# Optimization experiments

Measured on AMD Instinct MI355X. Metric: run time of the kernel, lower is better.

Reference implementation:

```python
import jax, jax.numpy as jnp
import numpy as np


def setup_inputs() -> dict:
    key = jax.random.key(0)
    k1, k2, k3, k4, k5 = jax.random.split(key, 5)
    N, M, K = 200000, 50, 4
    T = 1000.0
    ti = jnp.sort(jax.random.uniform(k1, (N,), dtype=jnp.float32) * T)
    mi = jax.random.randint(k2, (N,), 0, M, dtype=jnp.int64)
    mu_at_events = jax.random.uniform(k3, (N,), dtype=jnp.float32) * 0.5 + 0.05
    alpha = jax.random.uniform(k4, (K, M, M), dtype=jnp.float32) * 0.1
    gamma = jax.random.uniform(k5, (K,), dtype=jnp.float32) * 2.0 + 0.5
    return {"ti": ti, "mi": mi, "mu_at_events": mu_at_events, "alpha": alpha, "gamma": gamma}


def _hawkes_logsum(ti, mi, mu_at_events, alpha, gamma):
    # ti: [N] sorted event times; mi: [N] event types in [0, M)
    # alpha: [K, M, M]; gamma: [K]; mu_at_events: [N]
    N = ti.shape[0]
    M = alpha.shape[1]
    # inter-event gaps; dt[0] = 0 so the first event has zero excitation state
    dt = jnp.concatenate([jnp.zeros((1,), ti.dtype), ti[1:] - ti[:-1]])  # [N]
    a = jnp.exp(-gamma[None, :] * dt[:, None])  # [N, K] decay factors
    # one-hot of the PREVIOUS event's type (row 0 is all-zero, matching e_mi)
    prev_onehot = jnp.zeros((N, M), ti.dtype).at[jnp.arange(1, N), mi[:-1]].set(1.0)
    b = a[:, None, :] * prev_onehot[:, :, None]  # [N, M, K]

    # linear recurrence S_i = a_i * S_{i-1} + b_i via associative scan
    # combine((a1,b1),(a2,b2)) = (a1*a2, a2*b1 + b2)
    def combine(x, y):
        a1, b1 = x
        a2, b2 = y
        return (a1 * a2, a2[:, None, :] * b1 + b2)

    _, S = jax.lax.associative_scan(combine, (a, b))  # S: [N, M, K]
    # S[i, m, k] = sum_{j < i, m_j = m} exp(-gamma_k (t_i - t_j))
    alpha_at = alpha[:, mi, :]  # [K, N, M] rows of alpha for each event's type
    lam = mu_at_events + jnp.einsum('knm,nmk,k->n', alpha_at, S, gamma)  # [N]
    return jnp.sum(jnp.log(lam))


def reference(ti, mi, mu_at_events, alpha, gamma):
    return _hawkes_logsum(ti, mi, mu_at_events, alpha, gamma)
```

## Files before the change

### kernel.cpp

```cpp
#include <hip/hip_runtime.h>

#define CHUNK 256
#define MM 50
#define KK 4
#define STATE (MM*KK)
#define ASTRIDE 51
#define SUP 32
#define NSMAX 26
#define SUBSZ 32
#define GMAX 1024

__device__ int      g_ticket;
__device__ unsigned g_flag[GMAX];
__device__ unsigned g_sflag[64];
__device__ float    g_chunkB[GMAX * STATE];
__device__ float    g_superB[64 * STATE];

__device__ __forceinline__ unsigned short f2bf(float x) {
  unsigned u = __float_as_uint(x);
  u += 0x7fffu + ((u >> 16) & 1u);
  return (unsigned short)(u >> 16);
}
__device__ __forceinline__ float bflo(unsigned u) { return __uint_as_float(u << 16); }
__device__ __forceinline__ float bfhi(unsigned u) { return __uint_as_float(u & 0xffff0000u); }

__device__ __forceinline__ void st_agent(float* p, float v) {
  __hip_atomic_store(p, v, __ATOMIC_RELAXED, __HIP_MEMORY_SCOPE_AGENT);
}
__device__ __forceinline__ float ld_agent(const float* p) {
  return __hip_atomic_load(p, __ATOMIC_RELAXED, __HIP_MEMORY_SCOPE_AGENT);
}
__device__ __forceinline__ void spin_flag(unsigned* p, unsigned want) {
  while (__hip_atomic_load(p, __ATOMIC_RELAXED, __HIP_MEMORY_SCOPE_AGENT) != want)
    __builtin_amdgcn_s_sleep(2);
}

__global__ __launch_bounds__(512) void hawkes_fused(
    const float* __restrict__ ti, const int* __restrict__ mi,
    const float* __restrict__ mu, const float* __restrict__ alpha,
    const float* __restrict__ gamma, float* __restrict__ out,
    int N, int G, int NB) {
  int tid = threadIdx.x;
  __shared__ int vid_s;
  __shared__ uint2 P[MM * ASTRIDE];
  __shared__ __align__(16) float4 Fj[2 * CHUNK];
  __shared__ int   cj[2 * CHUNK];
  __shared__ __align__(16) float Q[16][STATE];
  __shared__ float red8[8];
  __shared__ float teL[SUP];
  __shared__ float tlast[NSMAX];
  __shared__ float SldsA[STATE];
  __shared__ float SldsB[STATE];
  __shared__ __align__(16) float RA[MM * 20];
  __shared__ __align__(16) float RB[MM * 20];

  if (tid == 0) vid_s = atomicAdd(&g_ticket, 1);

  int b = blockIdx.x;
  int gA = 2 * b, gB = gA + 1;
  bool hasB = (gB < G);
  int lA = gA * CHUNK;
  int sup = gA / SUP;
  int g0c = sup * SUP;
  int half = tid >> 8;
  int cidx = tid & 255;

  float gk0 = gamma[0], gk1 = gamma[1], gk2 = gamma[2], gk3 = gamma[3];
  float gkc = (tid & 2) ? ((tid & 1) ? gk3 : gk2) : ((tid & 1) ? gk1 : gk0);

  for (int i = tid; i < 16 * STATE; i += 512) ((float*)Q)[i] = 0.f;

  if (tid < SUP) {
    int c = g0c + tid;
    if (c < G) teL[tid] = ti[min(N, (c + 1) * CHUNK) - 1];
  } else if (tid >= 64 && tid < 64 + NSMAX) {
    int s = tid - 64;
    if (s < sup) tlast[s] = ti[min(N, (s + 1) * SUP * CHUNK) - 1];
  }

  float t_refA = ti[(gA == 0) ? 0 : (lA - 1)];
  float t_refB = ti[min(N, lA + CHUNK) - 1];
  float t_ref = half ? t_refB : t_refA;

  int j = lA - 1 + tid;
  int rX = min(N, lA + (half + 1) * CHUNK);
  bool valid = (j >= 0) && (j <= rX - 2);
  int myc = 0;
  float4 myF = make_float4(0.f, 0.f, 0.f, 0.f);
  if (valid) {
    myc = mi[j];
    float tj = ti[j] - t_ref;
    myF = make_float4(__expf(gk0 * tj), __expf(gk1 * tj),
                      __expf(gk2 * tj), __expf(gk3 * tj));
  }
  cj[tid] = myc;
  Fj[tid] = myF;
  __syncthreads();

  if (valid) {
    float* q = &Q[tid >> 5][myc * KK];
    atomicAdd(q + 0, myF.x); atomicAdd(q + 1, myF.y);
    atomicAdd(q + 2, myF.z); atomicAdd(q + 3, myF.w);
  }
  __syncthreads();

  bool sumr = (cidx < STATE) && (half == 0 || hasB);
  int gX = half ? gB : gA;
  float Bv = 0.f, dX = 0.f;
  if (sumr) {
    float tot = 0.f;
    #pragma unroll
    for (int q = 0; q < 8; ++q) tot += Q[half * 8 + q][cidx];
    dX = __expf(-gkc * (teL[gX - g0c] - t_ref));
    Bv = dX * tot;
    st_agent(&g_chunkB[(size_t)gX * STATE + cidx], Bv);
    float run = 0.f;
    #pragma unroll
    for (int q = 0; q < 8; ++q) {
      float tq = Q[half * 8 + q][cidx];
      Q[half * 8 + q][cidx] = run;
      run += tq;
    }
  }
  if (b == 0 && tid == 0) st_agent(out, 0.f);
  __syncthreads();
  unsigned DONE = (unsigned)(vid_s / NB) + 1u;
  if (tid == 0) {
    asm volatile("s_waitcnt vmcnt(0)" ::: "memory");
    __hip_atomic_store(&g_flag[gA], DONE, __ATOMIC_RELAXED, __HIP_MEMORY_SCOPE_AGENT);
    if (hasB)
      __hip_atomic_store(&g_flag[gB], DONE, __ATOMIC_RELAXED, __HIP_MEMORY_SCOPE_AGENT);
  }

  for (int idx = tid; idx < MM * MM; idx += 512) {
    int c = idx / MM, cp = idx - c * MM;
    float a0 = gk0 * alpha[idx];
    float a1 = gk1 * alpha[2500 + idx];
    float a2 = gk2 * alpha[5000 + idx];
    float a3 = gk3 * alpha[7500 + idx];
    P[c * ASTRIDE + cp] =
        make_uint2((unsigned)f2bf(a0) | ((unsigned)f2bf(a1) << 16),
                   (unsigned)f2bf(a2) | ((unsigned)f2bf(a3) << 16));
  }

  int n = lA + tid;
  bool en = (n < N);
  int c_n = en ? mi[n] : 0;
  float tn = 0.f, mun = 0.f;
  if (en) { tn = ti[n] - t_ref; mun = mu[n]; }

  int nlocA = gA - g0c;
  bool closer = (hasB && (gB - g0c == SUP - 1)) || (b == NB - 1);
  float S = 0.f;

  if (closer) {
    if (tid < nlocA) spin_flag(&g_flag[g0c + tid], DONE);
    __syncthreads();
    if (tid < STATE) {
      #pragma unroll 16
      for (int u = 0; u < nlocA; ++u)
        S += __expf(-gkc * (t_refA - teL[u])) * ld_agent(&g_chunkB[(size_t)(g0c + u) * STATE + tid]);
      SldsB[tid] = dX * S + Bv;
    }
    __syncthreads();
    if (sumr && half) {
      st_agent(&g_superB[(size_t)sup * STATE + cidx], dX * SldsB[cidx] + Bv);
    }
    __syncthreads();
    if (tid == 0) {
      asm volatile("s_waitcnt vmcnt(0)" ::: "memory");
      __hip_atomic_store(&g_sflag[sup], DONE, __ATOMIC_RELAXED, __HIP_MEMORY_SCOPE_AGENT);
    }
  }
  __syncthreads();

  float4 acc = make_float4(0.f, 0.f, 0.f, 0.f);
  if (en) {
    int rowb = c_n * ASTRIDE;
    const float4* wb = (const float4*)&Q[tid >> 5][0];
    if (cidx >= SUBSZ) {
      #pragma unroll 10
      for (int m = 0; m < MM; ++m) {
        uint2 p = P[rowb + m];
        float4 w = wb[m];
        acc.x += bflo(p.x) * w.x; acc.y += bfhi(p.x) * w.y;
        acc.z += bflo(p.y) * w.z; acc.w += bfhi(p.y) * w.w;
      }
    }
    int base = tid & ~(SUBSZ - 1);
    #pragma unroll 4
    for (int s = base; s <= tid; ++s) {
      uint2 p = P[rowb + cj[s]];
      float4 f = Fj[s];
      acc.x += bflo(p.x) * f.x; acc.y += bfhi(p.x) * f.y;
      acc.z += bflo(p.y) * f.z; acc.w += bfhi(p.y) * f.w;
    }
  }

  if (!closer) {
    if (tid < nlocA) spin_flag(&g_flag[g0c + tid], DONE);
    __syncthreads();
    if (tid < STATE) {
      #pragma unroll 16
      for (int u = 0; u < nlocA; ++u)
        S += __expf(-gkc * (t_refA - teL[u])) * ld_agent(&g_chunkB[(size_t)(g0c + u) * STATE + tid]);
    }
  }
  if (tid < sup) spin_flag(&g_sflag[tid], DONE);
  __syncthreads();
  if (tid < STATE) {
    #pragma unroll 16
    for (int s = 0; s < sup; ++s)
      S += __expf(-gkc * (t_refA - tlast[s])) * ld_agent(&g_superB[(size_t)s * STATE + tid]);
    SldsA[tid] = S;
    SldsB[tid] = dX * S + Bv;
  }
  __syncthreads();

  if (sumr) {
    int c = cidx >> 2, k = cidx & 3;
    const float* Sx = half ? SldsB : SldsA;
    float rv = 0.f;
    #pragma unroll 10
    for (int m = 0; m < MM; ++m) {
      uint2 p = P[c * ASTRIDE + m];
      unsigned w = (k & 2) ? p.y : p.x;
      float pv = (k & 1) ? bfhi(w) : bflo(w);
      rv += pv * Sx[m * KK + k];
    }
    (half ? RB : RA)[c * 20 + k] = rv;
  }
  __syncthreads();

  float local = 0.f;
  if (en) {
    const float* Rx = half ? RB : RA;
    float4 rv = *(const float4*)&Rx[c_n * 20];
    float lam = mun
              + __expf(-gk0 * tn) * (acc.x + rv.x)
              + __expf(-gk1 * tn) * (acc.y + rv.y)
              + __expf(-gk2 * tn) * (acc.z + rv.z)
              + __expf(-gk3 * tn) * (acc.w + rv.w);
    local = __logf(lam);
  }
  #pragma unroll
  for (int off = 32; off > 0; off >>= 1)
    local += __shfl_down(local, off, 64);
  if ((tid & 63) == 0) red8[tid >> 6] = local;
  __syncthreads();
  if (tid == 0) {
    float acc8 = 0.f;
    #pragma unroll
    for (int w = 0; w < 8; ++w) acc8 += red8[w];
    atomicAdd(out, acc8);
  }
}

extern "C" void kernel_launch(void* const* d_in, const int* in_sizes, int n_in,
                              void* d_out, int out_size, void* d_ws, size_t ws_size,
                              hipStream_t stream) {
  const float* ti    = (const float*)d_in[0];
  const int*   mi    = (const int*)d_in[1];
  const float* mu    = (const float*)d_in[2];
  const float* alpha = (const float*)d_in[3];
  const float* gamma = (const float*)d_in[4];
  float* out = (float*)d_out;
  int N = in_sizes[0];
  int G = (N + CHUNK - 1) / CHUNK;
  if (G > GMAX) return;
  int NB = (G + 1) / 2;

  hawkes_fused<<<NB, 512, 0, stream>>>(ti, mi, mu, alpha, gamma, out, N, G, NB);
}
```

Baseline: 88.70 us.

## Process four chunks per block with two events per thread

Each 512-thread block now handles four 256-event chunks instead of two, with every thread processing two events. The in-block chunk prefix is chained serially through shared memory, which halves the block count and the number of cross-block flag handshakes in the decoupled lookback. In exchange each block does more serial work and uses more LDS and registers, which may cut occupancy and parallelism (about 196 blocks for 256 CUs).

```diff
diff --git a/kernel.cpp b/kernel.cpp
--- a/kernel.cpp
+++ b/kernel.cpp
@@ -3,11 +3,11 @@
 #define CHUNK 256
 #define MM 50
 #define KK 4
-#define STATE (MM*KK)
+#define STATE 200
 #define ASTRIDE 51
 #define SUP 32
 #define NSMAX 26
-#define SUBSZ 32
+#define QUAD 4
 #define GMAX 1024
 
 __device__ int      g_ticket;
@@ -35,7 +35,7 @@
     __builtin_amdgcn_s_sleep(2);
 }
 
-__global__ __launch_bounds__(512) void hawkes_fused(
+__global__ __launch_bounds__(512) void hawkes_quad(
     const float* __restrict__ ti, const int* __restrict__ mi,
     const float* __restrict__ mu, const float* __restrict__ alpha,
     const float* __restrict__ gamma, float* __restrict__ out,
@@ -43,32 +43,29 @@
   int tid = threadIdx.x;
   __shared__ int vid_s;
   __shared__ uint2 P[MM * ASTRIDE];
-  __shared__ __align__(16) float4 Fj[2 * CHUNK];
-  __shared__ int   cj[2 * CHUNK];
-  __shared__ __align__(16) float Q[16][STATE];
-  __shared__ float red8[8];
+  __shared__ __align__(16) float4 Fj[4 * CHUNK];
+  __shared__ int   cj[4 * CHUNK];
+  __shared__ __align__(16) float Q[32][STATE];
+  __shared__ float BvL[QUAD][STATE];
+  __shared__ float Slds[QUAD][STATE];
+  __shared__ __align__(16) float RQ[QUAD][MM * 20];
   __shared__ float teL[SUP];
   __shared__ float tlast[NSMAX];
-  __shared__ float SldsA[STATE];
-  __shared__ float SldsB[STATE];
-  __shared__ __align__(16) float RA[MM * 20];
-  __shared__ __align__(16) float RB[MM * 20];
+  __shared__ float red8[8];
 
   if (tid == 0) vid_s = atomicAdd(&g_ticket, 1);
 
   int b = blockIdx.x;
-  int gA = 2 * b, gB = gA + 1;
-  bool hasB = (gB < G);
-  int lA = gA * CHUNK;
-  int sup = gA / SUP;
+  int c0 = b * QUAD;
+  int lQ = c0 * CHUNK;
+  int nEx = min(QUAD, G - c0);
+  int sup = b >> 3;
   int g0c = sup * SUP;
-  int half = tid >> 8;
-  int cidx = tid & 255;
+  int nloc = c0 - g0c;
 
   float gk0 = gamma[0], gk1 = gamma[1], gk2 = gamma[2], gk3 = gamma[3];
-  float gkc = (tid & 2) ? ((tid & 1) ? gk3 : gk2) : ((tid & 1) ? gk1 : gk0);
-
-  for (int i = tid; i < 16 * STATE; i += 512) ((float*)Q)[i] = 0.f;
+
+  for (int i = tid; i < 32 * STATE; i += 512) ((float*)Q)[i] = 0.f;
 
   if (tid < SUP) {
     int c = g0c + tid;
@@ -78,48 +75,62 @@
     if (s < sup) tlast[s] = ti[min(N, (s + 1) * SUP * CHUNK) - 1];
   }
 
-  float t_refA = ti[(gA == 0) ? 0 : (lA - 1)];
-  float t_refB = ti[min(N, lA + CHUNK) - 1];
-  float t_ref = half ? t_refB : t_refA;
-
-  int j = lA - 1 + tid;
-  int rX = min(N, lA + (half + 1) * CHUNK);
-  bool valid = (j >= 0) && (j <= rX - 2);
-  int myc = 0;
-  float4 myF = make_float4(0.f, 0.f, 0.f, 0.f);
-  if (valid) {
-    myc = mi[j];
-    float tj = ti[j] - t_ref;
-    myF = make_float4(__expf(gk0 * tj), __expf(gk1 * tj),
+  float tref0 = ti[(b == 0) ? 0 : (lQ - 1)];
+
+  int   myc[2]; float4 myF[2]; bool vld[2]; float trefE[2];
+  #pragma unroll
+  for (int ev = 0; ev < 2; ++ev) {
+    int slot = tid + 512 * ev;
+    int ch = slot >> 8;
+    int j = lQ - 1 + slot;
+    int rch = min(N, lQ + (ch + 1) * CHUNK);
+    int tri = (b == 0 && ch == 0) ? 0 : (lQ + ch * CHUNK - 1);
+    trefE[ev] = ti[min(N - 1, tri)];
+    bool v = (j >= 0) && (j <= rch - 2);
+    int c = 0; float4 F = make_float4(0.f, 0.f, 0.f, 0.f);
+    if (v) {
+      c = mi[j];
+      float tj = ti[j] - trefE[ev];
+      F = make_float4(__expf(gk0 * tj), __expf(gk1 * tj),
                       __expf(gk2 * tj), __expf(gk3 * tj));
-  }
-  cj[tid] = myc;
-  Fj[tid] = myF;
-  __syncthreads();
-
-  if (valid) {
-    float* q = &Q[tid >> 5][myc * KK];
-    atomicAdd(q + 0, myF.x); atomicAdd(q + 1, myF.y);
-    atomicAdd(q + 2, myF.z); atomicAdd(q + 3, myF.w);
-  }
-  __syncthreads();
-
-  bool sumr = (cidx < STATE) && (half == 0 || hasB);
-  int gX = half ? gB : gA;
-  float Bv = 0.f, dX = 0.f;
-  if (sumr) {
-    float tot = 0.f;
-    #pragma unroll
-    for (int q = 0; q < 8; ++q) tot += Q[half * 8 + q][cidx];
-    dX = __expf(-gkc * (teL[gX - g0c] - t_ref));
-    Bv = dX * tot;
-    st_agent(&g_chunkB[(size_t)gX * STATE + cidx], Bv);
-    float run = 0.f;
-    #pragma unroll
-    for (int q = 0; q < 8; ++q) {
-      float tq = Q[half * 8 + q][cidx];
-      Q[half * 8 + q][cidx] = run;
-      run += tq;
+    }
+    myc[ev] = c; myF[ev] = F; vld[ev] = v;
+    cj[slot] = c; Fj[slot] = F;
+  }
+  __syncthreads();
+
+  #pragma unroll
+  for (int ev = 0; ev < 2; ++ev) {
+    if (vld[ev]) {
+      int slot = tid + 512 * ev;
+      float* q = &Q[slot >> 5][myc[ev] * KK];
+      atomicAdd(q + 0, myF[ev].x); atomicAdd(q + 1, myF[ev].y);
+      atomicAdd(q + 2, myF[ev].z); atomicAdd(q + 3, myF[ev].w);
+    }
+  }
+  __syncthreads();
+
+  #pragma unroll
+  for (int half = 0; half < 2; ++half) {
+    int it = tid + 512 * half;
+    int ch = it >> 8, st = it & 255;
+    if (st < STATE && ch < nEx) {
+      float gkc = (st & 2) ? ((st & 1) ? gk3 : gk2) : ((st & 1) ? gk1 : gk0);
+      float trefc = (ch == 0) ? tref0 : teL[nloc + ch - 1];
+      float d = __expf(-gkc * (teL[nloc + ch] - trefc));
+      float tot = 0.f;
+      #pragma unroll
+      for (int q = 0; q < 8; ++q) tot += Q[8 * ch + q][st];
+      float Bv = d * tot;
+      st_agent(&g_chunkB[(size_t)(c0 + ch) * STATE + st], Bv);
+      BvL[ch][st] = Bv;
+      float run = 0.f;
+      #pragma unroll
+      for (int q = 0; q < 8; ++q) {
+        float tq = Q[8 * ch + q][st];
+        Q[8 * ch + q][st] = run;
+        run += tq;
+      }
     }
   }
   if (b == 0 && tid == 0) st_agent(out, 0.f);
@@ -127,9 +138,8 @@
   unsigned DONE = (unsigned)(vid_s / NB) + 1u;
   if (tid == 0) {
     asm volatile("s_waitcnt vmcnt(0)" ::: "memory");
-    __hip_atomic_store(&g_flag[gA], DONE, __ATOMIC_RELAXED, __HIP_MEMORY_SCOPE_AGENT);
-    if (hasB)
-      __hip_atomic_store(&g_flag[gB], DONE, __ATOMIC_RELAXED, __HIP_MEMORY_SCOPE_AGENT);
+    for (int ch = 0; ch < nEx; ++ch)
+      __hip_atomic_store(&g_flag[c0 + ch], DONE, __ATOMIC_RELAXED, __HIP_MEMORY_SCOPE_AGENT);
   }
 
   for (int idx = tid; idx < MM * MM; idx += 512) {
@@ -142,29 +152,34 @@
         make_uint2((unsigned)f2bf(a0) | ((unsigned)f2bf(a1) << 16),
                    (unsigned)f2bf(a2) | ((unsigned)f2bf(a3) << 16));
   }
-
-  int n = lA + tid;
-  bool en = (n < N);
-  int c_n = en ? mi[n] : 0;
-  float tn = 0.f, mun = 0.f;
-  if (en) { tn = ti[n] - t_ref; mun = mu[n]; }
-
-  int nlocA = gA - g0c;
-  bool closer = (hasB && (gB - g0c == SUP - 1)) || (b == NB - 1);
-  float S = 0.f;
+  int cn[2]; float tnv[2], muv[2]; bool en[2];
+  #pragma unroll
+  for (int ev = 0; ev < 2; ++ev) {
+    int n = lQ + tid + 512 * ev;
+    en[ev] = (n < N);
+    cn[ev] = en[ev] ? mi[n] : 0;
+    tnv[ev] = en[ev] ? (ti[n] - trefE[ev]) : 0.f;
+    muv[ev] = en[ev] ? mu[n] : 0.f;
+  }
+
+  bool closer = ((b & 7) == 7 && nEx == QUAD) || (b == NB - 1);
+  float gkc2 = (tid & 2) ? ((tid & 1) ? gk3 : gk2) : ((tid & 1) ? gk1 : gk0);
+  float S0 = 0.f;
 
   if (closer) {
-    if (tid < nlocA) spin_flag(&g_flag[g0c + tid], DONE);
+    if (tid < nloc) spin_flag(&g_flag[g0c + tid], DONE);
     __syncthreads();
     if (tid < STATE) {
-      #pragma unroll 16
-      for (int u = 0; u < nlocA; ++u)
-        S += __expf(-gkc * (t_refA - teL[u])) * ld_agent(&g_chunkB[(size_t)(g0c + u) * STATE + tid]);
-      SldsB[tid] = dX * S + Bv;
-    }
-    __syncthreads();
-    if (sumr && half) {
-      st_agent(&g_superB[(size_t)sup * STATE + cidx], dX * SldsB[cidx] + Bv);
+      #pragma unroll 14
+      for (int u = 0; u < nloc; ++u)
+        S0 += __expf(-gkc2 * (tref0 - teL[u])) * ld_agent(&g_chunkB[(size_t)(g0c + u) * STATE + tid]);
+      float s = S0;
+      for (int ch = 0; ch < nEx; ++ch) {
+        float trefc = (ch == 0) ? tref0 : teL[nloc + ch - 1];
+        float d = __expf(-gkc2 * (teL[nloc + ch] - trefc));
+        s = d * s + BvL[ch][tid];
+      }
+      st_agent(&g_superB[(size_t)sup * STATE + tid], s);
     }
     __syncthreads();
     if (tid == 0) {
@@ -174,74 +189,93 @@
   }
   __syncthreads();
 
-  float4 acc = make_float4(0.f, 0.f, 0.f, 0.f);
-  if (en) {
-    int rowb = c_n * ASTRIDE;
-    const float4* wb = (const float4*)&Q[tid >> 5][0];
-    if (cidx >= SUBSZ) {
+  float4 acc[2];
+  #pragma unroll
+  for (int ev = 0; ev < 2; ++ev) {
+    int slot = tid + 512 * ev;
+    float4 a = make_float4(0.f, 0.f, 0.f, 0.f);
+    if (en[ev]) {
+      int rowb = cn[ev] * ASTRIDE;
+      const float4* wb = (const float4*)&Q[slot >> 5][0];
+      if ((slot & 255) >= 32) {
+        #pragma unroll 10
+        for (int m = 0; m < MM; ++m) {
+          uint2 p = P[rowb + m];
+          float4 w = wb[m];
+          a.x += bflo(p.x) * w.x; a.y += bfhi(p.x) * w.y;
+          a.z += bflo(p.y) * w.z; a.w += bfhi(p.y) * w.w;
+        }
+      }
+      int base = slot & ~31;
+      #pragma unroll 4
+      for (int s = base; s <= slot; ++s) {
+        uint2 p = P[rowb + cj[s]];
+        float4 f = Fj[s];
+        a.x += bflo(p.x) * f.x; a.y += bfhi(p.x) * f.y;
+        a.z += bflo(p.y) * f.z; a.w += bfhi(p.y) * f.w;
+      }
+    }
+    acc[ev] = a;
+  }
+
+  if (!closer) {
+    if (tid < nloc) spin_flag(&g_flag[g0c + tid], DONE);
+    __syncthreads();
+    if (tid < STATE) {
+      #pragma unroll 14
+      for (int u = 0; u < nloc; ++u)
+        S0 += __expf(-gkc2 * (tref0 - teL[u])) * ld_agent(&g_chunkB[(size_t)(g0c + u) * STATE + tid]);
+    }
+  }
+  if (tid < sup) spin_flag(&g_sflag[tid], DONE);
+  __syncthreads();
+  if (tid < STATE) {
+    #pragma unroll 12
+    for (int s = 0; s < sup; ++s)
+      S0 += __expf(-gkc2 * (tref0 - tlast[s])) * ld_agent(&g_superB[(size_t)s * STATE + tid]);
+    float s = S0;
+    #pragma unroll
+    for (int ch = 0; ch < QUAD; ++ch) {
+      Slds[ch][tid] = s;
+      float trefc = (ch == 0) ? tref0 : teL[nloc + ch - 1];
+      float d = __expf(-gkc2 * (teL[nloc + ch] - trefc));
+      s = d * s + BvL[ch][tid];
+    }
+  }
+  __syncthreads();
+
+  #pragma unroll
+  for (int half = 0; half < 2; ++half) {
+    int it = tid + 512 * half;
+    int ch = it >> 8, st = it & 255;
+    if (st < STATE && ch < nEx) {
+      int c = st >> 2, k = st & 3;
+      float rv = 0.f;
       #pragma unroll 10
       for (int m = 0; m < MM; ++m) {
-        uint2 p = P[rowb + m];
-        float4 w = wb[m];
-        acc.x += bflo(p.x) * w.x; acc.y += bfhi(p.x) * w.y;
-        acc.z += bflo(p.y) * w.z; acc.w += bfhi(p.y) * w.w;
-      }
-    }
-    int base = tid & ~(SUBSZ - 1);
-    #pragma unroll 4
-    for (int s = base; s <= tid; ++s) {
-      uint2 p = P[rowb + cj[s]];
-      float4 f = Fj[s];
-      acc.x += bflo(p.x) * f.x; acc.y += bfhi(p.x) * f.y;
-      acc.z += bflo(p.y) * f.z; acc.w += bfhi(p.y) * f.w;
-    }
-  }
-
-  if (!closer) {
-    if (tid < nlocA) spin_flag(&g_flag[g0c + tid], DONE);
-    __syncthreads();
-    if (tid < STATE) {
-      #pragma unroll 16
-      for (int u = 0; u < nlocA; ++u)
-        S += __expf(-gkc * (t_refA - teL[u])) * ld_agent(&g_chunkB[(size_t)(g0c + u) * STATE + tid]);
-    }
-  }
-  if (tid < sup) spin_flag(&g_sflag[tid], DONE);
-  __syncthreads();
-  if (tid < STATE) {
-    #pragma unroll 16
-    for (int s = 0; s < sup; ++s)
-      S += __expf(-gkc * (t_refA - tlast[s])) * ld_agent(&g_superB[(size_t)s * STATE + tid]);
-    SldsA[tid] = S;
-    SldsB[tid] = dX * S + Bv;
-  }
-  __syncthreads();
-
-  if (sumr) {
-    int c = cidx >> 2, k = cidx & 3;
-    const float* Sx = half ? SldsB : SldsA;
-    float rv = 0.f;
-    #pragma unroll 10
-    for (int m = 0; m < MM; ++m) {
-      uint2 p = P[c * ASTRIDE + m];
-      unsigned w = (k & 2) ? p.y : p.x;
-      float pv = (k & 1) ? bfhi(w) : bflo(w);
-      rv += pv * Sx[m * KK + k];
-    }
-    (half ? RB : RA)[c * 20 + k] = rv;
+        uint2 p = P[c * ASTRIDE + m];
+        unsigned w = (k & 2) ? p.y : p.x;
+        float pv = (k & 1) ? bfhi(w) : bflo(w);
+        rv += pv * Slds[ch][m * KK + k];
+      }
+      RQ[ch][c * 20 + k] = rv;
+    }
   }
   __syncthreads();
 
   float local = 0.f;
-  if (en) {
-    const float* Rx = half ? RB : RA;
-    float4 rv = *(const float4*)&Rx[c_n * 20];
-    float lam = mun
-              + __expf(-gk0 * tn) * (acc.x + rv.x)
-              + __expf(-gk1 * tn) * (acc.y + rv.y)
-              + __expf(-gk2 * tn) * (acc.z + rv.z)
-              + __expf(-gk3 * tn) * (acc.w + rv.w);
-    local = __logf(lam);
+  #pragma unroll
+  for (int ev = 0; ev < 2; ++ev) {
+    if (en[ev]) {
+      int ch = (tid + 512 * ev) >> 8;
+      float4 rv = *(const float4*)&RQ[ch][cn[ev] * 20];
+      float lam = muv[ev]
+                + __expf(-gk0 * tnv[ev]) * (acc[ev].x + rv.x)
+                + __expf(-gk1 * tnv[ev]) * (acc[ev].y + rv.y)
+                + __expf(-gk2 * tnv[ev]) * (acc[ev].z + rv.z)
+                + __expf(-gk3 * tnv[ev]) * (acc[ev].w + rv.w);
+      local += __logf(lam);
+    }
   }
   #pragma unroll
   for (int off = 32; off > 0; off >>= 1)
@@ -268,7 +302,7 @@
   int N = in_sizes[0];
   int G = (N + CHUNK - 1) / CHUNK;
   if (G > GMAX) return;
-  int NB = (G + 1) / 2;
-
-  hawkes_fused<<<NB, 512, 0, stream>>>(ti, mi, mu, alpha, gamma, out, N, G, NB);
-}
+  int NB = (G + QUAD - 1) / QUAD;
+
+  hawkes_quad<<<NB, 512, 0, stream>>>(ti, mi, mu, alpha, gamma, out, N, G, NB);
+}
```

Measured after the change: 89.02 us. Within noise of the previous version (+0.4%).

## Replace flag-based cross-block scan handoff with epoch-signed data flags

Applied to the files above, without the earlier changes.

Removes the separate per-chunk and per-superchunk flag arrays. The chunk and superblock carry values themselves encode readiness: each is stored as sign(epoch)*(value+1), and consumers spin on the value. The carry state is folded into the Q prefix so the final lambda needs only one 50-term matvec, which replaces the separate R-matrix pass, and neighbour ti and mi come from wave shuffles. This is meant to cut flag stores, waitcnt fences, extra barriers and a matvec phase. The cost is a possible unsafe read ordering across relaxed atomics and per-element spin loops.

```diff
diff --git a/kernel.cpp b/kernel.cpp
--- a/kernel.cpp
+++ b/kernel.cpp
@@ -3,18 +3,15 @@
 #define CHUNK 256
 #define MM 50
 #define KK 4
-#define STATE (MM*KK)
+#define STATE 200
 #define ASTRIDE 51
 #define SUP 32
 #define NSMAX 26
-#define SUBSZ 32
 #define GMAX 1024
 
-__device__ int      g_ticket;
-__device__ unsigned g_flag[GMAX];
-__device__ unsigned g_sflag[64];
-__device__ float    g_chunkB[GMAX * STATE];
-__device__ float    g_superB[64 * STATE];
+__device__ int   g_ticket;
+__device__ float g_chunkB[GMAX * STATE];
+__device__ float g_superB[64 * STATE];
 
 __device__ __forceinline__ unsigned short f2bf(float x) {
   unsigned u = __float_as_uint(x);
@@ -30,12 +27,8 @@
 __device__ __forceinline__ float ld_agent(const float* p) {
   return __hip_atomic_load(p, __ATOMIC_RELAXED, __HIP_MEMORY_SCOPE_AGENT);
 }
-__device__ __forceinline__ void spin_flag(unsigned* p, unsigned want) {
-  while (__hip_atomic_load(p, __ATOMIC_RELAXED, __HIP_MEMORY_SCOPE_AGENT) != want)
-    __builtin_amdgcn_s_sleep(2);
-}
-
-__global__ __launch_bounds__(512) void hawkes_fused(
+
+__global__ __launch_bounds__(512) void hawkes_df(
     const float* __restrict__ ti, const int* __restrict__ mi,
     const float* __restrict__ mu, const float* __restrict__ alpha,
     const float* __restrict__ gamma, float* __restrict__ out,
@@ -43,33 +36,26 @@
   int tid = threadIdx.x;
   __shared__ int vid_s;
   __shared__ uint2 P[MM * ASTRIDE];
-  __shared__ __align__(16) float4 Fj[2 * CHUNK];
-  __shared__ int   cj[2 * CHUNK];
+  __shared__ __align__(16) float4 Fj[512];
+  __shared__ int   cj[512];
   __shared__ __align__(16) float Q[16][STATE];
-  __shared__ float red8[8];
   __shared__ float teL[SUP];
   __shared__ float tlast[NSMAX];
-  __shared__ float SldsA[STATE];
-  __shared__ float SldsB[STATE];
-  __shared__ __align__(16) float RA[MM * 20];
-  __shared__ __align__(16) float RB[MM * 20];
+  __shared__ float red8[8];
 
   if (tid == 0) vid_s = atomicAdd(&g_ticket, 1);
 
   int b = blockIdx.x;
-  int gA = 2 * b, gB = gA + 1;
-  bool hasB = (gB < G);
-  int lA = gA * CHUNK;
-  int sup = gA / SUP;
+  int c0 = 2 * b;
+  int lQ = c0 * CHUNK;
+  int sup = b >> 4;
   int g0c = sup * SUP;
-  int half = tid >> 8;
-  int cidx = tid & 255;
+  int nloc = c0 - g0c;
+  int ch = tid >> 8;
 
   float gk0 = gamma[0], gk1 = gamma[1], gk2 = gamma[2], gk3 = gamma[3];
-  float gkc = (tid & 2) ? ((tid & 1) ? gk3 : gk2) : ((tid & 1) ? gk1 : gk0);
 
   for (int i = tid; i < 16 * STATE; i += 512) ((float*)Q)[i] = 0.f;
-
   if (tid < SUP) {
     int c = g0c + tid;
     if (c < G) teL[tid] = ti[min(N, (c + 1) * CHUNK) - 1];
@@ -77,117 +63,69 @@
     int s = tid - 64;
     if (s < sup) tlast[s] = ti[min(N, (s + 1) * SUP * CHUNK) - 1];
   }
-
-  float t_refA = ti[(gA == 0) ? 0 : (lA - 1)];
-  float t_refB = ti[min(N, lA + CHUNK) - 1];
-  float t_ref = half ? t_refB : t_refA;
-
-  int j = lA - 1 + tid;
-  int rX = min(N, lA + (half + 1) * CHUNK);
-  bool valid = (j >= 0) && (j <= rX - 2);
-  int myc = 0;
-  float4 myF = make_float4(0.f, 0.f, 0.f, 0.f);
+  if (b == 0 && tid == 0) st_agent(out, 0.f);
+
+  float tref_ch = ti[(b == 0 && ch == 0) ? 0 : (lQ + ch * CHUNK - 1)];
+  int n = lQ + tid;
+  bool has_n = (n < N);
+  float ti_n = has_n ? ti[n] : 0.f;
+  int   mi_n = has_n ? mi[n] : 0;
+  float mu_n = has_n ? mu[n] : 0.f;
+  int j = lQ - 1 + tid;
+  float ti_j = __shfl_up(ti_n, 1, 64);
+  int   mi_j = __shfl_up(mi_n, 1, 64);
+  if ((tid & 63) == 0 && j >= 0) { ti_j = ti[j]; mi_j = mi[j]; }
+  bool valid = (j >= 0) && has_n;
+  int myc = valid ? mi_j : 0;
+  float4 F = make_float4(0.f, 0.f, 0.f, 0.f);
   if (valid) {
-    myc = mi[j];
-    float tj = ti[j] - t_ref;
-    myF = make_float4(__expf(gk0 * tj), __expf(gk1 * tj),
-                      __expf(gk2 * tj), __expf(gk3 * tj));
+    float tj = ti_j - tref_ch;
+    F = make_float4(__expf(gk0 * tj), __expf(gk1 * tj),
+                    __expf(gk2 * tj), __expf(gk3 * tj));
   }
   cj[tid] = myc;
-  Fj[tid] = myF;
+  Fj[tid] = F;
   __syncthreads();
 
   if (valid) {
     float* q = &Q[tid >> 5][myc * KK];
-    atomicAdd(q + 0, myF.x); atomicAdd(q + 1, myF.y);
-    atomicAdd(q + 2, myF.z); atomicAdd(q + 3, myF.w);
-  }
-  __syncthreads();
-
-  bool sumr = (cidx < STATE) && (half == 0 || hasB);
-  int gX = half ? gB : gA;
-  float Bv = 0.f, dX = 0.f;
-  if (sumr) {
-    float tot = 0.f;
-    #pragma unroll
-    for (int q = 0; q < 8; ++q) tot += Q[half * 8 + q][cidx];
-    dX = __expf(-gkc * (teL[gX - g0c] - t_ref));
-    Bv = dX * tot;
-    st_agent(&g_chunkB[(size_t)gX * STATE + cidx], Bv);
-    float run = 0.f;
-    #pragma unroll
-    for (int q = 0; q < 8; ++q) {
-      float tq = Q[half * 8 + q][cidx];
-      Q[half * 8 + q][cidx] = run;
-      run += tq;
-    }
-  }
-  if (b == 0 && tid == 0) st_agent(out, 0.f);
-  __syncthreads();
-  unsigned DONE = (unsigned)(vid_s / NB) + 1u;
-  if (tid == 0) {
-    asm volatile("s_waitcnt vmcnt(0)" ::: "memory");
-    __hip_atomic_store(&g_flag[gA], DONE, __ATOMIC_RELAXED, __HIP_MEMORY_SCOPE_AGENT);
-    if (hasB)
-      __hip_atomic_store(&g_flag[gB], DONE, __ATOMIC_RELAXED, __HIP_MEMORY_SCOPE_AGENT);
-  }
-
-  for (int idx = tid; idx < MM * MM; idx += 512) {
-    int c = idx / MM, cp = idx - c * MM;
-    float a0 = gk0 * alpha[idx];
-    float a1 = gk1 * alpha[2500 + idx];
-    float a2 = gk2 * alpha[5000 + idx];
-    float a3 = gk3 * alpha[7500 + idx];
-    P[c * ASTRIDE + cp] =
-        make_uint2((unsigned)f2bf(a0) | ((unsigned)f2bf(a1) << 16),
-                   (unsigned)f2bf(a2) | ((unsigned)f2bf(a3) << 16));
-  }
-
-  int n = lA + tid;
-  bool en = (n < N);
-  int c_n = en ? mi[n] : 0;
-  float tn = 0.f, mun = 0.f;
-  if (en) { tn = ti[n] - t_ref; mun = mu[n]; }
-
-  int nlocA = gA - g0c;
-  bool closer = (hasB && (gB - g0c == SUP - 1)) || (b == NB - 1);
-  float S = 0.f;
-
-  if (closer) {
-    if (tid < nlocA) spin_flag(&g_flag[g0c + tid], DONE);
-    __syncthreads();
-    if (tid < STATE) {
-      #pragma unroll 16
-      for (int u = 0; u < nlocA; ++u)
-        S += __expf(-gkc * (t_refA - teL[u])) * ld_agent(&g_chunkB[(size_t)(g0c + u) * STATE + tid]);
-      SldsB[tid] = dX * S + Bv;
-    }
-    __syncthreads();
-    if (sumr && half) {
-      st_agent(&g_superB[(size_t)sup * STATE + cidx], dX * SldsB[cidx] + Bv);
-    }
-    __syncthreads();
-    if (tid == 0) {
-      asm volatile("s_waitcnt vmcnt(0)" ::: "memory");
-      __hip_atomic_store(&g_sflag[sup], DONE, __ATOMIC_RELAXED, __HIP_MEMORY_SCOPE_AGENT);
-    }
-  }
-  __syncthreads();
+    atomicAdd(q + 0, F.x); atomicAdd(q + 1, F.y);
+    atomicAdd(q + 2, F.z); atomicAdd(q + 3, F.w);
+  }
+  #pragma unroll
+  for (int u = 0; u < 5; ++u) {
+    int idx = tid + 512 * u;
+    if (idx < MM * MM) {
+      int c = idx / MM, cp = idx - c * MM;
+      float a0 = gk0 * alpha[idx];
+      float a1 = gk1 * alpha[2500 + idx];
+      float a2 = gk2 * alpha[5000 + idx];
+      float a3 = gk3 * alpha[7500 + idx];
+      P[c * ASTRIDE + cp] =
+          make_uint2((unsigned)f2bf(a0) | ((unsigned)f2bf(a1) << 16),
+                     (unsigned)f2bf(a2) | ((unsigned)f2bf(a3) << 16));
+    }
+  }
+  __syncthreads();
+
+  float epoch_s = ((vid_s / NB) & 1) ? -1.f : 1.f;
+  float gkc = (tid & 2) ? ((tid & 1) ? gk3 : gk2) : ((tid & 1) ? gk1 : gk0);
+  float totA = 0.f, totB = 0.f, dA = 0.f, dB = 0.f;
+  if (tid < STATE) {
+    #pragma unroll
+    for (int q = 0; q < 8; ++q)  totA += Q[q][tid];
+    #pragma unroll
+    for (int q = 8; q < 16; ++q) totB += Q[q][tid];
+    dA = __expf(-gkc * (teL[nloc] - tref_ch));
+    dB = __expf(-gkc * (teL[nloc + 1] - teL[nloc]));
+    st_agent(&g_chunkB[(size_t)c0 * STATE + tid], epoch_s * (dA * totA + 1.f));
+    st_agent(&g_chunkB[(size_t)(c0 + 1) * STATE + tid], epoch_s * (dB * totB + 1.f));
+  }
 
   float4 acc = make_float4(0.f, 0.f, 0.f, 0.f);
-  if (en) {
-    int rowb = c_n * ASTRIDE;
-    const float4* wb = (const float4*)&Q[tid >> 5][0];
-    if (cidx >= SUBSZ) {
-      #pragma unroll 10
-      for (int m = 0; m < MM; ++m) {
-        uint2 p = P[rowb + m];
-        float4 w = wb[m];
-        acc.x += bflo(p.x) * w.x; acc.y += bfhi(p.x) * w.y;
-        acc.z += bflo(p.y) * w.z; acc.w += bfhi(p.y) * w.w;
-      }
-    }
-    int base = tid & ~(SUBSZ - 1);
+  if (has_n) {
+    int rowb = mi_n * ASTRIDE;
+    int base = tid & ~31;
     #pragma unroll 4
     for (int s = base; s <= tid; ++s) {
       uint2 p = P[rowb + cj[s]];
@@ -197,50 +135,76 @@
     }
   }
 
-  if (!closer) {
-    if (tid < nlocA) spin_flag(&g_flag[g0c + tid], DONE);
-    __syncthreads();
-    if (tid < STATE) {
-      #pragma unroll 16
-      for (int u = 0; u < nlocA; ++u)
-        S += __expf(-gkc * (t_refA - teL[u])) * ld_agent(&g_chunkB[(size_t)(g0c + u) * STATE + tid]);
-    }
-  }
-  if (tid < sup) spin_flag(&g_sflag[tid], DONE);
-  __syncthreads();
+  bool closer = ((b & 15) == 15) || (b == NB - 1);
+  float S = 0.f;
   if (tid < STATE) {
-    #pragma unroll 16
-    for (int s = 0; s < sup; ++s)
-      S += __expf(-gkc * (t_refA - tlast[s])) * ld_agent(&g_superB[(size_t)s * STATE + tid]);
-    SldsA[tid] = S;
-    SldsB[tid] = dX * S + Bv;
-  }
-  __syncthreads();
-
-  if (sumr) {
-    int c = cidx >> 2, k = cidx & 3;
-    const float* Sx = half ? SldsB : SldsA;
-    float rv = 0.f;
+    for (int u0 = 0; u0 < nloc; u0 += 16) {
+      float r[16];
+      #pragma unroll
+      for (int u = 0; u < 16; ++u)
+        r[u] = (u0 + u < nloc)
+             ? ld_agent(&g_chunkB[(size_t)(g0c + u0 + u) * STATE + tid])
+             : epoch_s;
+      #pragma unroll
+      for (int u = 0; u < 16; ++u) {
+        if (u0 + u < nloc) {
+          float v = r[u];
+          while (epoch_s * v < 0.5f) {
+            __builtin_amdgcn_s_sleep(1);
+            v = ld_agent(&g_chunkB[(size_t)(g0c + u0 + u) * STATE + tid]);
+          }
+          S += __expf(-gkc * (tref_ch - teL[u0 + u])) * (epoch_s * v - 1.f);
+        }
+      }
+    }
+    if (closer) {
+      float run2 = dA * (S + totA);
+      run2 = dB * (run2 + totB);
+      st_agent(&g_superB[(size_t)sup * STATE + tid], epoch_s * (run2 + 1.f));
+    }
+    for (int s0 = 0; s0 < sup; s0 += 16) {
+      float r[16];
+      #pragma unroll
+      for (int u = 0; u < 16; ++u)
+        r[u] = (s0 + u < sup)
+             ? ld_agent(&g_superB[(size_t)(s0 + u) * STATE + tid])
+             : epoch_s;
+      #pragma unroll
+      for (int u = 0; u < 16; ++u) {
+        if (s0 + u < sup) {
+          float v = r[u];
+          while (epoch_s * v < 0.5f) {
+            __builtin_amdgcn_s_sleep(1);
+            v = ld_agent(&g_superB[(size_t)(s0 + u) * STATE + tid]);
+          }
+          S += __expf(-gkc * (tref_ch - tlast[s0 + u])) * (epoch_s * v - 1.f);
+        }
+      }
+    }
+    float run = S;
+    #pragma unroll
+    for (int q = 0; q < 8; ++q)  { float t = Q[q][tid]; Q[q][tid] = run; run += t; }
+    run = dA * run;
+    #pragma unroll
+    for (int q = 8; q < 16; ++q) { float t = Q[q][tid]; Q[q][tid] = run; run += t; }
+  }
+  __syncthreads();
+
+  float local = 0.f;
+  if (has_n) {
+    int rowb = mi_n * ASTRIDE;
+    const float4* wb = (const float4*)&Q[tid >> 5][0];
     #pragma unroll 10
     for (int m = 0; m < MM; ++m) {
-      uint2 p = P[c * ASTRIDE + m];
-      unsigned w = (k & 2) ? p.y : p.x;
-      float pv = (k & 1) ? bfhi(w) : bflo(w);
-      rv += pv * Sx[m * KK + k];
-    }
-    (half ? RB : RA)[c * 20 + k] = rv;
-  }
-  __syncthreads();
-
-  float local = 0.f;
-  if (en) {
-    const float* Rx = half ? RB : RA;
-    float4 rv = *(const float4*)&Rx[c_n * 20];
-    float lam = mun
-              + __expf(-gk0 * tn) * (acc.x + rv.x)
-              + __expf(-gk1 * tn) * (acc.y + rv.y)
-              + __expf(-gk2 * tn) * (acc.z + rv.z)
-              + __expf(-gk3 * tn) * (acc.w + rv.w);
+      uint2 p = P[rowb + m];
+      float4 w = wb[m];
+      acc.x += bflo(p.x) * w.x; acc.y += bfhi(p.x) * w.y;
+      acc.z += bflo(p.y) * w.z; acc.w += bfhi(p.y) * w.w;
+    }
+    float tn = ti_n - tref_ch;
+    float lam = mu_n
+              + __expf(-gk0 * tn) * acc.x + __expf(-gk1 * tn) * acc.y
+              + __expf(-gk2 * tn) * acc.z + __expf(-gk3 * tn) * acc.w;
     local = __logf(lam);
   }
   #pragma unroll
@@ -270,5 +234,5 @@
   if (G > GMAX) return;
   int NB = (G + 1) / 2;
 
-  hawkes_fused<<<NB, 512, 0, stream>>>(ti, mi, mu, alpha, gamma, out, N, G, NB);
-}
+  hawkes_df<<<NB, 512, 0, stream>>>(ti, mi, mu, alpha, gamma, out, N, G, NB);
+}
```

After: 86.39 us. 1.03x faster.
